# Optimization experiments

Hardware: AMD Instinct MI355X
Metric: run time of the kernel (lower is better)

The kernel has to match this reference:

```python
import jax, jax.numpy as jnp
import numpy as np

N = 524288      # number of spacetime samples (rays*samples)
E = 16          # num_experts
K = 2           # num_selected_experts
HID = 16        # SpacetimeGeometricMLP hidden_dim (layers are hidden_dim*2 wide)
OUT = 4         # rgb + density


def setup_inputs() -> dict:
    key = jax.random.key(0)
    ks = jax.random.split(key, 8)
    return {
        "xyzt": jax.random.normal(ks[0], (N, 4), jnp.float32),
        # gate: Linear(4, E)
        "Wg": jax.random.normal(ks[1], (4, E), jnp.float32) * 0.5,
        "bg": jnp.zeros((E,), jnp.float32),
        # per-expert SphericalEmbedding params
        "proj": jax.random.normal(ks[2], (E, 3, 8), jnp.float32),
        "center": jax.random.normal(ks[3], (E, 3), jnp.float32) * 0.01,
        # per-expert TimeEmbedding biases
        "tb1": jnp.zeros((E,), jnp.float32),
        "tb2": jnp.zeros((E,), jnp.float32),
        # per-expert feature_mlp Linear(12, 2*HID, bias=False) and final Linear(2*HID, OUT)
        "W1": jax.random.normal(ks[4], (E, 12, 2 * HID), jnp.float32) * (12 ** -0.5),
        "Wf": jax.random.normal(ks[5], (E, 2 * HID, OUT), jnp.float32) * ((2 * HID) ** -0.5),
        "bf": jnp.zeros((E, OUT), jnp.float32),
    }


def _moe_forward(xyzt, Wg, bg, proj, center, tb1, tb2, W1, Wf, bf):
    n = xyzt.shape[0]
    # --- gate: top-k + softmax over selected logits (softmax in fp32, as in torch) ---
    logits = xyzt @ Wg + bg                                   # [N, E]
    w, sel = jax.lax.top_k(logits, K)                         # [N, K]
    w = jax.nn.softmax(w.astype(jnp.float32), axis=1).astype(xyzt.dtype)
    # dense combine weights: zero for unselected experts -> identical math to
    # the torch gather/scatter loop with sum pooling.
    w_dense = jnp.zeros((n, E), xyzt.dtype).at[jnp.arange(n)[:, None], sel].set(w)  # [N, E]

    xyz, t = xyzt[:, :3], xyzt[:, 3:4]

    def expert(proj_e, center_e, tb1_e, tb2_e, W1_e, Wf_e, bf_e):
        # SphericalEmbedding
        xc = xyz - center_e                                   # [N, 3]
        rho = jnp.sqrt(jnp.sum(xc * xc, -1, keepdims=True))   # [N, 1]
        phi = jnp.arctan2(xc[:, 1], xc[:, 0])[:, None]
        theta = jnp.arccos(xc[:, 2] / (rho[:, 0] + 1e-6))[:, None]
        sph = jnp.concatenate([rho, phi, theta], -1) @ proj_e  # [N, 8]
        # TimeEmbedding
        cos_t = jnp.cos(t + tb1_e)
        sin_t = jnp.sin(t + tb2_e)
        temb = jnp.concatenate([cos_t, sin_t, jax.nn.silu(cos_t), jax.nn.silu(sin_t)], -1)  # [N, 4]
        emb = jnp.concatenate([sph, temb], -1)                # [N, 12]
        # feature_mlp (depth=0, no bias) + final_layer
        h = emb @ W1_e                                        # [N, 2*HID]
        return h @ Wf_e + bf_e                                # [N, OUT]

    outs = jax.vmap(expert)(proj, center, tb1, tb2, W1, Wf, bf)  # [E, N, OUT]
    return jnp.einsum('ne,end->nd', w_dense, outs)               # [N, OUT]


def reference(xyzt, Wg, bg, proj, center, tb1, tb2, W1, Wf, bf):
    return _moe_forward(xyzt, Wg, bg, proj, center, tb1, tb2, W1, Wf, bf)
```

## Files before the change

kernel.cpp:

```cpp
#include <hip/hip_runtime.h>
#include <math.h>

#define NE 16
#define WPE 44


__global__ __launch_bounds__(256) void moe_prep_kernel(
        const float* __restrict__ proj,
        const float* __restrict__ center,
        const float* __restrict__ tb1,
        const float* __restrict__ tb2,
        const float* __restrict__ W1,
        const float* __restrict__ Wf,
        const float* __restrict__ bf,
        float* __restrict__ tbl) {
    __shared__ float Msh[NE * 48];
    int t = threadIdx.x;
    {
        int e = t >> 4, l = t & 15;
        #pragma unroll
        for (int k = 0; k < 3; ++k) {
            int j = l + k * 16;
            int i = j >> 2, d = j & 3;
            const float* w1r = W1 + (e * 12 + i) * 32;
            const float* wfc = Wf + e * 128 + d;
            float s = 0.f;
            #pragma unroll
            for (int q = 0; q < 32; ++q) s = fmaf(w1r[q], wfc[q * 4], s);
            Msh[e * 48 + j] = s;
        }
    }
    __syncthreads();
    if (t < NE * 4) {
        int e = t >> 2, d = t & 3;
        const float* Me = Msh + e * 48;
        float* o = tbl + e * WPE;
        #pragma unroll
        for (int j = 0; j < 3; ++j) {
            float s = 0.f;
            const float* pr = proj + e * 24 + j * 8;
            #pragma unroll
            for (int i = 0; i < 8; ++i) s = fmaf(pr[i], Me[i * 4 + d], s);
            o[j * 4 + d] = s;
        }
        #pragma unroll
        for (int i = 0; i < 4; ++i) o[(3 + i) * 4 + d] = Me[(8 + i) * 4 + d];
        o[7 * 4 + d] = bf[e * 4 + d];
        if (d == 0) {
            o[32] = center[e * 3 + 0];
            o[33] = center[e * 3 + 1];
            o[34] = center[e * 3 + 2];
            o[35] = cosf(tb1[e]);
            o[36] = sinf(tb1[e]);
            o[37] = cosf(tb2[e]);
            o[38] = sinf(tb2[e]);
            o[39] = 0.f; o[40] = 0.f; o[41] = 0.f; o[42] = 0.f; o[43] = 0.f;
        }
    }
}

__device__ __forceinline__ float fast_rcp(float x) {
    return __builtin_amdgcn_rcpf(x);
}

__device__ __forceinline__ float4 f4fma(float s, float4 a, float4 b) {
    return make_float4(fmaf(s, a.x, b.x), fmaf(s, a.y, b.y),
                       fmaf(s, a.z, b.z), fmaf(s, a.w, b.w));
}

__device__ __forceinline__ float fast_atan2f(float y, float x) {
    float ax = fabsf(x), ay = fabsf(y);
    float mx = fmaxf(ax, ay), mn = fminf(ax, ay);
    float r = mn * fast_rcp(fmaxf(mx, 1e-37f));
    float s = r * r;
    float p =              -0.0117212f;
    p = fmaf(p, s,  0.05265332f);
    p = fmaf(p, s, -0.11643287f);
    p = fmaf(p, s,  0.19354346f);
    p = fmaf(p, s, -0.33262347f);
    p = fmaf(p, s,  0.99997726f);
    float a = r * p;
    a = (ay > ax) ? (1.57079637f - a) : a;
    a = (x < 0.f) ? (3.14159274f - a) : a;
    return copysignf(a, y);
}

__device__ __forceinline__ float fast_acosf(float x) {
    float ax = fminf(fabsf(x), 1.f);
    float p = fmaf(ax, -0.0187293f, 0.0742610f);
    p = fmaf(p, ax, -0.2121144f);
    p = fmaf(p, ax, 1.5707288f);
    float r = sqrtf(1.f - ax) * p;
    return (x >= 0.f) ? r : (3.14159274f - r);
}

__global__ __launch_bounds__(256) void moe_main_kernel(
        const float4* __restrict__ xyzt,
        const float* __restrict__ Wg,
        const float* __restrict__ bg,
        const float* __restrict__ tbl,
        float4* __restrict__ out, int n) {
    __shared__ float lds[NE * WPE];
    for (int i = threadIdx.x; i < NE * WPE; i += 256) lds[i] = tbl[i];
    __syncthreads();

    int idx = blockIdx.x * 256 + threadIdx.x;
    if (idx >= n) return;
    float4 p = xyzt[idx];

    float logits[NE];
    #pragma unroll
    for (int e = 0; e < NE; ++e) {
        logits[e] = fmaf(p.x, Wg[e],
                    fmaf(p.y, Wg[NE + e],
                    fmaf(p.z, Wg[2 * NE + e],
                    fmaf(p.w, Wg[3 * NE + e], bg[e]))));
    }
    float best = logits[0]; int bi = 0;
    float second = -INFINITY; int si = 0;
    #pragma unroll
    for (int e = 1; e < NE; ++e) {
        float l = logits[e];
        if (l > best)        { second = best; si = bi; best = l; bi = e; }
        else if (l > second) { second = l; si = e; }
    }
    float ed = __expf(second - best);
    float w0 = fast_rcp(1.f + ed);
    float w1 = ed * w0;

    float st, ct;
    __sincosf(p.w, &st, &ct);

    int   sel[2] = { bi, si };
    float wgt[2] = { w0, w1 };
    float4 acc = make_float4(0.f, 0.f, 0.f, 0.f);

    #pragma unroll
    for (int kk = 0; kk < 2; ++kk) {
        const float4* w4 = (const float4*)(lds + sel[kk] * WPE);
        float4 cc = w4[8];
        float4 ss = w4[9];
        float xc0 = p.x - cc.x, xc1 = p.y - cc.y, xc2 = p.z - cc.z;
        float rho = sqrtf(fmaf(xc0, xc0, fmaf(xc1, xc1, xc2 * xc2)));
        float phi = fast_atan2f(xc1, xc0);
        float theta = fast_acosf(xc2 * fast_rcp(rho + 1e-6f));
        float cos_t = fmaf(ct, cc.w, -st * ss.x);
        float sin_t = fmaf(st, ss.y,  ct * ss.z);
        float silc = cos_t * fast_rcp(1.f + __expf(-cos_t));
        float sils = sin_t * fast_rcp(1.f + __expf(-sin_t));

        float4 r = w4[7];
        r = f4fma(rho,   w4[0], r);
        r = f4fma(phi,   w4[1], r);
        r = f4fma(theta, w4[2], r);
        r = f4fma(cos_t, w4[3], r);
        r = f4fma(sin_t, w4[4], r);
        r = f4fma(silc,  w4[5], r);
        r = f4fma(sils,  w4[6], r);
        acc = f4fma(wgt[kk], r, acc);
    }
    out[idx] = acc;
}

extern "C" void kernel_launch(void* const* d_in, const int* in_sizes, int n_in,
                              void* d_out, int out_size, void* d_ws, size_t ws_size,
                              hipStream_t stream) {
    const float* xyzt   = (const float*)d_in[0];
    const float* Wg     = (const float*)d_in[1];
    const float* bg     = (const float*)d_in[2];
    const float* proj   = (const float*)d_in[3];
    const float* center = (const float*)d_in[4];
    const float* tb1    = (const float*)d_in[5];
    const float* tb2    = (const float*)d_in[6];
    const float* W1     = (const float*)d_in[7];
    const float* Wf     = (const float*)d_in[8];
    const float* bf     = (const float*)d_in[9];
    float* tbl = (float*)d_ws;
    int n = in_sizes[0] / 4;

    moe_prep_kernel<<<1, 256, 0, stream>>>(proj, center, tb1, tb2, W1, Wf, bf, tbl);
    moe_main_kernel<<<(n + 255) / 256, 256, 0, stream>>>(
        (const float4*)xyzt, Wg, bg, tbl, (float4*)d_out, n);
}
```

Baseline: 87.24 us.

## Fuse expert weight-folding prep into main kernel, per-block recompute

Removes the separate single-block prep kernel and has every block recompute the folded per-expert table (W1·Wf, proj fold, trig of time biases) in shared memory before processing its samples. Each block now handles two chunks of 256 samples to amortise that setup. This removes one kernel launch and its serial dependency, at the cost of redundant per-block loads of W1/Wf (about 14 KB) and extra LDS use, which may lower occupancy.

```diff
diff --git a/kernel.cpp b/kernel.cpp
--- a/kernel.cpp
+++ b/kernel.cpp
@@ -3,61 +3,11 @@
 
 #define NE 16
 #define WPE 44
-
-
-__global__ __launch_bounds__(256) void moe_prep_kernel(
-        const float* __restrict__ proj,
-        const float* __restrict__ center,
-        const float* __restrict__ tb1,
-        const float* __restrict__ tb2,
-        const float* __restrict__ W1,
-        const float* __restrict__ Wf,
-        const float* __restrict__ bf,
-        float* __restrict__ tbl) {
-    __shared__ float Msh[NE * 48];
-    int t = threadIdx.x;
-    {
-        int e = t >> 4, l = t & 15;
-        #pragma unroll
-        for (int k = 0; k < 3; ++k) {
-            int j = l + k * 16;
-            int i = j >> 2, d = j & 3;
-            const float* w1r = W1 + (e * 12 + i) * 32;
-            const float* wfc = Wf + e * 128 + d;
-            float s = 0.f;
-            #pragma unroll
-            for (int q = 0; q < 32; ++q) s = fmaf(w1r[q], wfc[q * 4], s);
-            Msh[e * 48 + j] = s;
-        }
-    }
-    __syncthreads();
-    if (t < NE * 4) {
-        int e = t >> 2, d = t & 3;
-        const float* Me = Msh + e * 48;
-        float* o = tbl + e * WPE;
-        #pragma unroll
-        for (int j = 0; j < 3; ++j) {
-            float s = 0.f;
-            const float* pr = proj + e * 24 + j * 8;
-            #pragma unroll
-            for (int i = 0; i < 8; ++i) s = fmaf(pr[i], Me[i * 4 + d], s);
-            o[j * 4 + d] = s;
-        }
-        #pragma unroll
-        for (int i = 0; i < 4; ++i) o[(3 + i) * 4 + d] = Me[(8 + i) * 4 + d];
-        o[7 * 4 + d] = bf[e * 4 + d];
-        if (d == 0) {
-            o[32] = center[e * 3 + 0];
-            o[33] = center[e * 3 + 1];
-            o[34] = center[e * 3 + 2];
-            o[35] = cosf(tb1[e]);
-            o[36] = sinf(tb1[e]);
-            o[37] = cosf(tb2[e]);
-            o[38] = sinf(tb2[e]);
-            o[39] = 0.f; o[40] = 0.f; o[41] = 0.f; o[42] = 0.f; o[43] = 0.f;
-        }
-    }
-}
+#define CHUNKS 2
+
+#define W1S 36
+#define WFS 36
+
 
 __device__ __forceinline__ float fast_rcp(float x) {
     return __builtin_amdgcn_rcpf(x);
@@ -94,72 +44,164 @@
     return (x >= 0.f) ? r : (3.14159274f - r);
 }
 
-__global__ __launch_bounds__(256) void moe_main_kernel(
+__global__ __launch_bounds__(256) void moe_fused_kernel(
         const float4* __restrict__ xyzt,
         const float* __restrict__ Wg,
         const float* __restrict__ bg,
-        const float* __restrict__ tbl,
+        const float* __restrict__ proj,
+        const float* __restrict__ center,
+        const float* __restrict__ tb1,
+        const float* __restrict__ tb2,
+        const float* __restrict__ W1,
+        const float* __restrict__ Wf,
+        const float* __restrict__ bf,
         float4* __restrict__ out, int n) {
-    __shared__ float lds[NE * WPE];
-    for (int i = threadIdx.x; i < NE * WPE; i += 256) lds[i] = tbl[i];
+    __shared__ __align__(16) union {
+        float w1[NE * 12 * W1S];
+        float tbl[NE * WPE];
+    } U;
+    __shared__ __align__(16) float WfT[NE * 4 * WFS];
+    __shared__ float Msh[NE * 48];
+
+    int t = threadIdx.x;
+
+    {
+        const float4* g4 = (const float4*)W1;
+        float4* s4 = (float4*)U.w1;
+        #pragma unroll
+        for (int it = 0; it < 6; ++it) {
+            int i4 = t + it * 256;
+            int row = i4 >> 3, c = i4 & 7;
+            s4[row * (W1S / 4) + c] = g4[i4];
+        }
+    }
+    {
+        const float4* g4 = (const float4*)Wf;
+        #pragma unroll
+        for (int it = 0; it < 2; ++it) {
+            int i4 = t + it * 256;
+            int e = i4 >> 5, q = i4 & 31;
+            float4 v = g4[i4];
+            WfT[(e * 4 + 0) * WFS + q] = v.x;
+            WfT[(e * 4 + 1) * WFS + q] = v.y;
+            WfT[(e * 4 + 2) * WFS + q] = v.z;
+            WfT[(e * 4 + 3) * WFS + q] = v.w;
+        }
+    }
     __syncthreads();
 
-    int idx = blockIdx.x * 256 + threadIdx.x;
-    if (idx >= n) return;
-    float4 p = xyzt[idx];
-
-    float logits[NE];
+    {
+        int e = t >> 4, l = t & 15;
+        int d = l & 3, i0 = l >> 2;
+        const float4* col = (const float4*)(WfT + (e * 4 + d) * WFS);
+        float4 cv[8];
+        #pragma unroll
+        for (int c = 0; c < 8; ++c) cv[c] = col[c];
+        #pragma unroll
+        for (int k = 0; k < 3; ++k) {
+            int i = i0 + k * 4;
+            const float4* rowp = (const float4*)(U.w1 + (e * 12 + i) * W1S);
+            float s = 0.f;
+            #pragma unroll
+            for (int c = 0; c < 8; ++c) {
+                float4 r = rowp[c];
+                s = fmaf(r.x, cv[c].x, s);
+                s = fmaf(r.y, cv[c].y, s);
+                s = fmaf(r.z, cv[c].z, s);
+                s = fmaf(r.w, cv[c].w, s);
+            }
+            Msh[e * 48 + i * 4 + d] = s;
+        }
+    }
+    __syncthreads();
+
+    if (t < NE * 4) {
+        int e = t >> 2, d = t & 3;
+        const float* Me = Msh + e * 48;
+        float* o = U.tbl + e * WPE;
+        #pragma unroll
+        for (int j = 0; j < 3; ++j) {
+            float s = 0.f;
+            const float* pr = proj + e * 24 + j * 8;
+            #pragma unroll
+            for (int i = 0; i < 8; ++i) s = fmaf(pr[i], Me[i * 4 + d], s);
+            o[j * 4 + d] = s;
+        }
+        #pragma unroll
+        for (int i = 0; i < 4; ++i) o[(3 + i) * 4 + d] = Me[(8 + i) * 4 + d];
+        o[7 * 4 + d] = bf[e * 4 + d];
+        if (d == 0) {
+            o[32] = center[e * 3 + 0];
+            o[33] = center[e * 3 + 1];
+            o[34] = center[e * 3 + 2];
+            o[35] = cosf(tb1[e]);
+            o[36] = sinf(tb1[e]);
+            o[37] = cosf(tb2[e]);
+            o[38] = sinf(tb2[e]);
+            o[39] = 0.f; o[40] = 0.f; o[41] = 0.f; o[42] = 0.f; o[43] = 0.f;
+        }
+    }
+    __syncthreads();
+
     #pragma unroll
-    for (int e = 0; e < NE; ++e) {
-        logits[e] = fmaf(p.x, Wg[e],
-                    fmaf(p.y, Wg[NE + e],
-                    fmaf(p.z, Wg[2 * NE + e],
-                    fmaf(p.w, Wg[3 * NE + e], bg[e]))));
-    }
-    float best = logits[0]; int bi = 0;
-    float second = -INFINITY; int si = 0;
-    #pragma unroll
-    for (int e = 1; e < NE; ++e) {
-        float l = logits[e];
-        if (l > best)        { second = best; si = bi; best = l; bi = e; }
-        else if (l > second) { second = l; si = e; }
-    }
-    float ed = __expf(second - best);
-    float w0 = fast_rcp(1.f + ed);
-    float w1 = ed * w0;
-
-    float st, ct;
-    __sincosf(p.w, &st, &ct);
-
-    int   sel[2] = { bi, si };
-    float wgt[2] = { w0, w1 };
-    float4 acc = make_float4(0.f, 0.f, 0.f, 0.f);
-
-    #pragma unroll
-    for (int kk = 0; kk < 2; ++kk) {
-        const float4* w4 = (const float4*)(lds + sel[kk] * WPE);
-        float4 cc = w4[8];
-        float4 ss = w4[9];
-        float xc0 = p.x - cc.x, xc1 = p.y - cc.y, xc2 = p.z - cc.z;
-        float rho = sqrtf(fmaf(xc0, xc0, fmaf(xc1, xc1, xc2 * xc2)));
-        float phi = fast_atan2f(xc1, xc0);
-        float theta = fast_acosf(xc2 * fast_rcp(rho + 1e-6f));
-        float cos_t = fmaf(ct, cc.w, -st * ss.x);
-        float sin_t = fmaf(st, ss.y,  ct * ss.z);
-        float silc = cos_t * fast_rcp(1.f + __expf(-cos_t));
-        float sils = sin_t * fast_rcp(1.f + __expf(-sin_t));
-
-        float4 r = w4[7];
-        r = f4fma(rho,   w4[0], r);
-        r = f4fma(phi,   w4[1], r);
-        r = f4fma(theta, w4[2], r);
-        r = f4fma(cos_t, w4[3], r);
-        r = f4fma(sin_t, w4[4], r);
-        r = f4fma(silc,  w4[5], r);
-        r = f4fma(sils,  w4[6], r);
-        acc = f4fma(wgt[kk], r, acc);
-    }
-    out[idx] = acc;
+    for (int c2 = 0; c2 < CHUNKS; ++c2) {
+        int idx = (blockIdx.x * CHUNKS + c2) * 256 + t;
+        if (idx >= n) continue;
+        float4 p = xyzt[idx];
+
+        float logits[NE];
+        #pragma unroll
+        for (int e = 0; e < NE; ++e) {
+            logits[e] = fmaf(p.x, Wg[e],
+                        fmaf(p.y, Wg[NE + e],
+                        fmaf(p.z, Wg[2 * NE + e],
+                        fmaf(p.w, Wg[3 * NE + e], bg[e]))));
+        }
+        float best = logits[0]; int bi = 0;
+        float second = -INFINITY; int si = 0;
+        #pragma unroll
+        for (int e = 1; e < NE; ++e) {
+            float l = logits[e];
+            if (l > best)        { second = best; si = bi; best = l; bi = e; }
+            else if (l > second) { second = l; si = e; }
+        }
+        float ed = __expf(second - best);
+        float w0 = fast_rcp(1.f + ed);
+        float w1 = ed * w0;
+
+        float st, ct;
+        __sincosf(p.w, &st, &ct);
+
+        int   sel[2] = { bi, si };
+        float wgt[2] = { w0, w1 };
+        float4 acc = make_float4(0.f, 0.f, 0.f, 0.f);
+
+        #pragma unroll
+        for (int kk = 0; kk < 2; ++kk) {
+            const float4* w4 = (const float4*)(U.tbl + sel[kk] * WPE);
+            float4 cc = w4[8];
+            float4 ss = w4[9];
+            float xc0 = p.x - cc.x, xc1 = p.y - cc.y, xc2 = p.z - cc.z;
+            float rho = sqrtf(fmaf(xc0, xc0, fmaf(xc1, xc1, xc2 * xc2)));
+            float phi = fast_atan2f(xc1, xc0);
+            float theta = fast_acosf(xc2 * fast_rcp(rho + 1e-6f));
+            float cos_t = fmaf(ct, cc.w, -st * ss.x);
+            float sin_t = fmaf(st, ss.y,  ct * ss.z);
+            float silc = cos_t * fast_rcp(1.f + __expf(-cos_t));
+            float sils = sin_t * fast_rcp(1.f + __expf(-sin_t));
+
+            float4 r = w4[7];
+            r = f4fma(rho,   w4[0], r);
+            r = f4fma(phi,   w4[1], r);
+            r = f4fma(theta, w4[2], r);
+            r = f4fma(cos_t, w4[3], r);
+            r = f4fma(sin_t, w4[4], r);
+            r = f4fma(silc,  w4[5], r);
+            r = f4fma(sils,  w4[6], r);
+            acc = f4fma(wgt[kk], r, acc);
+        }
+        out[idx] = acc;
+    }
 }
 
 extern "C" void kernel_launch(void* const* d_in, const int* in_sizes, int n_in,
@@ -175,10 +217,11 @@
     const float* W1     = (const float*)d_in[7];
     const float* Wf     = (const float*)d_in[8];
     const float* bf     = (const float*)d_in[9];
-    float* tbl = (float*)d_ws;
+    (void)d_ws; (void)ws_size;
     int n = in_sizes[0] / 4;
 
-    moe_prep_kernel<<<1, 256, 0, stream>>>(proj, center, tb1, tb2, W1, Wf, bf, tbl);
-    moe_main_kernel<<<(n + 255) / 256, 256, 0, stream>>>(
-        (const float4*)xyzt, Wg, bg, tbl, (float4*)d_out, n);
-}
+    int nblk = (n + 256 * CHUNKS - 1) / (256 * CHUNKS);
+    moe_fused_kernel<<<nblk, 256, 0, stream>>>(
+        (const float4*)xyzt, Wg, bg, proj, center, tb1, tb2, W1, Wf, bf,
+        (float4*)d_out, n);
+}
```

Result: faster. 83.31 us (-4.5%).
